# Kernel tuning notes

Measured on AMD Instinct MI355X. Metric: run time of the kernel, lower is better.

## Reference

```python
import jax, jax.numpy as jnp
import numpy as np

D_MODEL = 1024
N_HEADS = 16
HEAD_DIM = D_MODEL // N_HEADS


def setup_inputs() -> dict:
    key = jax.random.key(0)
    k1, k2, k3, k4, k5, k6 = jax.random.split(key, 6)
    B, T_q, T_kv = 4, 1024, 4096
    s = 1.0 / np.sqrt(D_MODEL)
    return {
        "query": jax.random.normal(k1, (B, T_q, D_MODEL), dtype=jnp.float32),
        "kv_source": jax.random.normal(k2, (B, T_kv, D_MODEL), dtype=jnp.float32),
        "w_q": jax.random.normal(k3, (D_MODEL, D_MODEL), dtype=jnp.float32) * s,
        "w_k": jax.random.normal(k4, (D_MODEL, D_MODEL), dtype=jnp.float32) * s,
        "w_v": jax.random.normal(k5, (D_MODEL, D_MODEL), dtype=jnp.float32) * s,
        "w_o": jax.random.normal(k6, (D_MODEL, D_MODEL), dtype=jnp.float32) * s,
    }


def reference(query, kv_source, w_q, w_k, w_v, w_o):
    B, T_q, _ = query.shape
    T_kv = kv_source.shape[1]
    # Linear(d,d,bias=False): y = x @ W^T
    q = (query @ w_q.T).reshape(B, T_q, N_HEADS, HEAD_DIM)
    k = (kv_source @ w_k.T).reshape(B, T_kv, N_HEADS, HEAD_DIM)
    v = (kv_source @ w_v.T).reshape(B, T_kv, N_HEADS, HEAD_DIM)
    scale = HEAD_DIM ** -0.5
    # scores: (B, H, T_q, T_kv)
    attn = jax.nn.softmax(jnp.einsum('bqhd,bkhd->bhqk', q, k) * scale, axis=-1)
    out = jnp.einsum('bhqk,bkhd->bqhd', attn, v).reshape(B, T_q, D_MODEL)
    return out @ w_o.T
```

## Files before the change

kernel.cpp:

```cpp
#include <hip/hip_runtime.h>
#include <hip/hip_bf16.h>


typedef __attribute__((ext_vector_type(4))) float f32x4;
typedef __attribute__((ext_vector_type(16))) float f32x16;
typedef __attribute__((ext_vector_type(8))) short bf16x8;

__device__ __forceinline__ unsigned short f2bf(float f) {
  unsigned u = __float_as_uint(f);
  u = (u + 0x7fffu + ((u >> 16) & 1u)) >> 16;
  return (unsigned short)u;
}

__device__ __forceinline__ void pl32swap(unsigned& x, unsigned& y) {
  asm volatile("v_permlane32_swap_b32 %0, %1" : "+v"(x), "+v"(y));
}

#define GLD_LDS16(g, l)                                                     \
  __builtin_amdgcn_global_load_lds(                                        \
      (const __attribute__((address_space(1))) unsigned int*)(const void*)(g), \
      (__attribute__((address_space(3))) unsigned int*)(void*)(l), 16, 0, 0)

__global__ void cvt_all(const float* __restrict__ q, const float* __restrict__ kv,
                        const float* __restrict__ wq, const float* __restrict__ wk,
                        const float* __restrict__ wv, const float* __restrict__ wo,
                        unsigned short* __restrict__ q_bf,
                        unsigned short* __restrict__ kv_bf,
                        unsigned short* __restrict__ wq_bf,
                        unsigned short* __restrict__ wk_bf,
                        unsigned short* __restrict__ wv_bf,
                        unsigned short* __restrict__ wo_bf) {
  const int QN = 4194304, KVN = 16777216, WN = 1048576;
  const float SC = 0.125f * 1.44269504088896f;
  int total_quads = (QN + KVN + 4 * WN) >> 2;
  int stride = gridDim.x * blockDim.x;
  for (int t = blockIdx.x * blockDim.x + threadIdx.x; t < total_quads; t += stride) {
    int i = t << 2;
    const float* src;
    unsigned short* dst;
    float sc = 1.0f;
    int off;
    if (i < QN) { src = q; dst = q_bf; off = i; }
    else if (i < QN + KVN) { src = kv; dst = kv_bf; off = i - QN; }
    else if (i < QN + KVN + WN) { src = wq; dst = wq_bf; off = i - QN - KVN; sc = SC; }
    else if (i < QN + KVN + 2 * WN) { src = wk; dst = wk_bf; off = i - QN - KVN - WN; }
    else if (i < QN + KVN + 3 * WN) { src = wv; dst = wv_bf; off = i - QN - KVN - 2 * WN; }
    else { src = wo; dst = wo_bf; off = i - QN - KVN - 3 * WN; }
    float4 v = *(const float4*)(src + off);
    ushort4 r;
    r.x = f2bf(v.x * sc); r.y = f2bf(v.y * sc);
    r.z = f2bf(v.z * sc); r.w = f2bf(v.w * sc);
    *(ushort4*)(dst + off) = r;
  }
}

template <int WRITE_BF16>
__global__ __launch_bounds__(256) void gemm_bt(
    const unsigned short* __restrict__ A, const unsigned short* __restrict__ Bt,
    void* __restrict__ Cp, int M, int N, int K, int ldc) {
  __shared__ __align__(16) unsigned short Ash[4096];
  __shared__ __align__(16) unsigned short Bsh[4096];

  int tiles_n = N >> 7;
  int nwg = gridDim.x;
  int wg = blockIdx.x;
  int cpx = nwg >> 3;
  wg = (wg & 7) * cpx + (wg >> 3);
  int tm = wg / tiles_n, tn = wg - tm * tiles_n;

  int tid = threadIdx.x;
  int lane = tid & 63, wave = tid >> 6;
  int wr = wave >> 1, wc = wave & 1;
  int brow = tm << 7, bcol = tn << 7;

  int fr = lane & 15, fg = lane >> 4;
  int swz = (fr >> 1) & 3;

  int srow = lane >> 2;
  int sg = (lane & 3) ^ ((srow >> 1) & 3);

  const unsigned short* aG0 = A + (size_t)(brow + wave * 32 + srow) * K + sg * 8;
  const unsigned short* aG1 = A + (size_t)(brow + wave * 32 + 16 + srow) * K + sg * 8;
  const unsigned short* bG0 = Bt + (size_t)(bcol + wave * 32 + srow) * K + sg * 8;
  const unsigned short* bG1 = Bt + (size_t)(bcol + wave * 32 + 16 + srow) * K + sg * 8;
  unsigned short* aL0 = Ash + wave * 1024;
  unsigned short* aL1 = Ash + wave * 1024 + 512;
  unsigned short* bL0 = Bsh + wave * 1024;
  unsigned short* bL1 = Bsh + wave * 1024 + 512;

  const f32x4 zero4 = {0.f, 0.f, 0.f, 0.f};
  f32x4 acc[4][4];
#pragma unroll
  for (int m = 0; m < 4; ++m)
#pragma unroll
    for (int n = 0; n < 4; ++n) acc[m][n] = zero4;

  for (int k0 = 0; k0 < K; k0 += 32) {
    GLD_LDS16(aG0 + k0, aL0);
    GLD_LDS16(aG1 + k0, aL1);
    GLD_LDS16(bG0 + k0, bL0);
    GLD_LDS16(bG1 + k0, bL1);
    __syncthreads();

    bf16x8 af[4], bfr[4];
#pragma unroll
    for (int m = 0; m < 4; ++m) {
      int r = wr * 64 + m * 16 + fr;
      af[m] = *(const bf16x8*)(Ash + r * 32 + ((fg ^ swz) * 8));
    }
#pragma unroll
    for (int n = 0; n < 4; ++n) {
      int r = wc * 64 + n * 16 + fr;
      bfr[n] = *(const bf16x8*)(Bsh + r * 32 + ((fg ^ swz) * 8));
    }
#pragma unroll
    for (int m = 0; m < 4; ++m)
#pragma unroll
      for (int n = 0; n < 4; ++n)
        acc[m][n] =
            __builtin_amdgcn_mfma_f32_16x16x32_bf16(af[m], bfr[n], acc[m][n], 0, 0, 0);
    __syncthreads();
  }

  int crow = brow + wr * 64 + fg * 4;
  int ccol = bcol + wc * 64 + fr;
#pragma unroll
  for (int m = 0; m < 4; ++m)
#pragma unroll
    for (int n = 0; n < 4; ++n)
#pragma unroll
      for (int j = 0; j < 4; ++j) {
        size_t off = (size_t)(crow + m * 16 + j) * ldc + (ccol + n * 16);
        if (WRITE_BF16)
          ((unsigned short*)Cp)[off] = f2bf(acc[m][n][j]);
        else
          ((float*)Cp)[off] = acc[m][n][j];
      }
}

__global__ __launch_bounds__(128) void attn_fwd(
    const unsigned short* __restrict__ qp,
    const unsigned short* __restrict__ kp,
    const unsigned short* __restrict__ vt,
    unsigned short* __restrict__ ao) {
  __shared__ __align__(16) unsigned short Ksh[128 * 64];
  __shared__ __align__(16) unsigned short Vsh[64 * 128];

  int idx = (blockIdx.x & 7) * 128 + (blockIdx.x >> 3);
  int qt = idx & 15;
  int h = (idx >> 4) & 15;
  int b = idx >> 8;
  int tid = threadIdx.x;
  int lane = tid & 63, w = tid >> 6;
  int q5 = lane & 31, hi = lane >> 5;

  const unsigned short* qptr =
      qp + (size_t)(b * 1024 + qt * 64 + w * 32 + q5) * 1024 + h * 64 + hi * 8;
  bf16x8 qf[4];
#pragma unroll
  for (int s = 0; s < 4; ++s) qf[s] = *(const bf16x8*)(qptr + s * 16);

  bf16x8 ones;
#pragma unroll
  for (int e = 0; e < 8; ++e) ones[e] = (short)0x3F80;

  f32x16 O[2], rsum;
#pragma unroll
  for (int r = 0; r < 16; ++r) { O[0][r] = 0.f; O[1][r] = 0.f; rsum[r] = 0.f; }
  float mrun = -1e30f;

  const unsigned short* kS[8];
#pragma unroll
  for (int i = 0; i < 8; ++i) {
    int row = w * 64 + i * 8 + (lane >> 3);
    int g = (lane & 7) ^ ((row ^ (2 * (row >> 3))) & 7);
    kS[i] = kp + (size_t)(b * 4096 + row) * 1024 + h * 64 + g * 8;
  }
  const unsigned short* vS[8];
#pragma unroll
  for (int i = 0; i < 8; ++i) {
    int row = w * 32 + i * 4 + (lane >> 4);
    int g = (lane & 15) ^ ((row >> 1) & 14);
    vS[i] = vt + (size_t)(h * 64 + row) * 16384 + b * 4096 + g * 8;
  }

  int xk = hi ^ ((q5 ^ (2 * (q5 >> 3))) & 7);
  int koff[4];
#pragma unroll
  for (int s = 0; s < 4; ++s) koff[s] = q5 * 64 + (((2 * s) ^ xk) * 8);
  int xv = hi ^ ((q5 >> 1) & 14);
  int voff[4][2];
#pragma unroll
  for (int kt = 0; kt < 4; ++kt)
#pragma unroll
    for (int p = 0; p < 2; ++p)
      voff[kt][p] = q5 * 128 + (((4 * kt + 2 * p) ^ xv) * 8);

  for (int it = 0; it < 32; ++it) {
#pragma unroll
    for (int i = 0; i < 8; ++i) GLD_LDS16(kS[i], Ksh + w * 4096 + i * 512);
#pragma unroll
    for (int i = 0; i < 8; ++i) GLD_LDS16(vS[i], Vsh + w * 4096 + i * 512);
#pragma unroll
    for (int i = 0; i < 8; ++i) { kS[i] += 131072; vS[i] += 128; }
    __syncthreads();

    f32x16 S[4];
#pragma unroll
    for (int kt = 0; kt < 4; ++kt)
#pragma unroll
      for (int r = 0; r < 16; ++r) S[kt][r] = 0.f;
    __builtin_amdgcn_s_setprio(1);
#pragma unroll
    for (int kt = 0; kt < 4; ++kt)
#pragma unroll
      for (int s = 0; s < 4; ++s) {
        bf16x8 kf = *(const bf16x8*)(Ksh + kt * 2048 + koff[s]);
        S[kt] = __builtin_amdgcn_mfma_f32_32x32x16_bf16(kf, qf[s], S[kt], 0, 0, 0);
      }
    __builtin_amdgcn_s_setprio(0);

    float t[16];
#pragma unroll
    for (int r = 0; r < 16; ++r)
      t[r] = fmaxf(fmaxf(S[0][r], S[1][r]), fmaxf(S[2][r], S[3][r]));
#pragma unroll
    for (int st = 8; st >= 1; st >>= 1)
#pragma unroll
      for (int r = 0; r < 8; ++r)
        if (r < st) t[r] = fmaxf(t[r], t[r + st]);
    float cmax = fmaxf(t[0], __shfl_xor(t[0], 32));

    if (__any(cmax > mrun)) {
      float mn = fmaxf(mrun, cmax);
      float fsc = exp2f(mrun - mn);
      mrun = mn;
#pragma unroll
      for (int r = 0; r < 16; ++r) {
        rsum[r] *= fsc; O[0][r] *= fsc; O[1][r] *= fsc;
      }
    }

#pragma unroll
    for (int kt = 0; kt < 4; ++kt) {
      float p[16];
#pragma unroll
      for (int r = 0; r < 16; ++r) p[r] = exp2f(S[kt][r] - mrun);
      unsigned u[8];
#pragma unroll
      for (int i = 0; i < 8; ++i) {
        __hip_bfloat162 pk = __float22bfloat162_rn(float2{p[2 * i], p[2 * i + 1]});
        u[i] = *reinterpret_cast<unsigned*>(&pk);
      }
      pl32swap(u[0], u[2]);
      pl32swap(u[1], u[3]);
      pl32swap(u[4], u[6]);
      pl32swap(u[5], u[7]);
      union PU { unsigned uu[4]; bf16x8 v; };
      PU a0; a0.uu[0] = u[0]; a0.uu[1] = u[1]; a0.uu[2] = u[2]; a0.uu[3] = u[3];
      PU a1; a1.uu[0] = u[4]; a1.uu[1] = u[5]; a1.uu[2] = u[6]; a1.uu[3] = u[7];
      bf16x8 pf0 = a0.v, pf1 = a1.v;

      __builtin_amdgcn_s_setprio(1);
      rsum = __builtin_amdgcn_mfma_f32_32x32x16_bf16(ones, pf0, rsum, 0, 0, 0);
      rsum = __builtin_amdgcn_mfma_f32_32x32x16_bf16(ones, pf1, rsum, 0, 0, 0);
#pragma unroll
      for (int dt = 0; dt < 2; ++dt) {
        bf16x8 vf0 = *(const bf16x8*)(Vsh + voff[kt][0] + dt * 4096);
        bf16x8 vf1 = *(const bf16x8*)(Vsh + voff[kt][1] + dt * 4096);
        O[dt] = __builtin_amdgcn_mfma_f32_32x32x16_bf16(vf0, pf0, O[dt], 0, 0, 0);
        O[dt] = __builtin_amdgcn_mfma_f32_32x32x16_bf16(vf1, pf1, O[dt], 0, 0, 0);
      }
      __builtin_amdgcn_s_setprio(0);
    }
    __syncthreads();
  }

  float inv = 1.0f / rsum[0];
  size_t obase = (size_t)(b * 1024 + qt * 64 + w * 32 + q5) * 1024 + h * 64;
#pragma unroll
  for (int dt = 0; dt < 2; ++dt)
#pragma unroll
    for (int j2 = 0; j2 < 4; ++j2) {
      ushort4 pk;
      pk.x = f2bf(O[dt][4 * j2 + 0] * inv);
      pk.y = f2bf(O[dt][4 * j2 + 1] * inv);
      pk.z = f2bf(O[dt][4 * j2 + 2] * inv);
      pk.w = f2bf(O[dt][4 * j2 + 3] * inv);
      *(ushort4*)(ao + obase + dt * 32 + j2 * 8 + hi * 4) = pk;
    }
}

extern "C" void kernel_launch(void* const* d_in, const int* in_sizes, int n_in,
                              void* d_out, int out_size, void* d_ws, size_t ws_size,
                              hipStream_t stream) {
  const float* query = (const float*)d_in[0];
  const float* kvs = (const float*)d_in[1];
  const float* wq = (const float*)d_in[2];
  const float* wk = (const float*)d_in[3];
  const float* wv = (const float*)d_in[4];
  const float* wo = (const float*)d_in[5];
  float* out = (float*)d_out;
  char* ws = (char*)d_ws;
  const size_t MB = 1ull << 20;

  unsigned short* q_bf = (unsigned short*)(ws + 0 * MB);
  unsigned short* kv_bf = (unsigned short*)(ws + 8 * MB);
  unsigned short* wq_bf = (unsigned short*)(ws + 40 * MB);
  unsigned short* wk_bf = (unsigned short*)(ws + 42 * MB);
  unsigned short* wv_bf = (unsigned short*)(ws + 44 * MB);
  unsigned short* wo_bf = (unsigned short*)(ws + 46 * MB);
  unsigned short* qp = (unsigned short*)(ws + 48 * MB);
  unsigned short* kp = (unsigned short*)(ws + 56 * MB);
  unsigned short* vt = (unsigned short*)(ws + 88 * MB);
  unsigned short* ao = (unsigned short*)(ws + 120 * MB);

  cvt_all<<<2048, 256, 0, stream>>>(query, kvs, wq, wk, wv, wo, q_bf, kv_bf,
                                    wq_bf, wk_bf, wv_bf, wo_bf);

  gemm_bt<1><<<256, 256, 0, stream>>>(q_bf, wq_bf, qp, 4096, 1024, 1024, 1024);
  gemm_bt<1><<<1024, 256, 0, stream>>>(kv_bf, wk_bf, kp, 16384, 1024, 1024, 1024);
  gemm_bt<1><<<1024, 256, 0, stream>>>(wv_bf, kv_bf, vt, 1024, 16384, 1024, 16384);

  attn_fwd<<<1024, 128, 0, stream>>>(qp, kp, vt, ao);

  gemm_bt<0><<<256, 256, 0, stream>>>(ao, wo_bf, out, 4096, 1024, 1024, 1024);
}
```

Measured before the change: 500.6 us.

## Split KV sequence across wave pairs in attention and merge partial softmax

The attention kernel now runs 4 waves per block instead of 2. Each pair of waves handles half of the KV sequence (split-K) for the same 64 queries, using 64-row KV tiles per iteration. The two partial softmax states are combined at the end through shared memory using the running max and sum. This raises occupancy and shortens the per-wave serial loop, at the cost of an extra LDS reduction and a barrier in the epilogue.

```diff
diff --git a/kernel.cpp b/kernel.cpp
--- a/kernel.cpp
+++ b/kernel.cpp
@@ -138,13 +138,14 @@
       }
 }
 
-__global__ __launch_bounds__(128) void attn_fwd(
+__global__ __launch_bounds__(256, 4) void attn_fwd(
     const unsigned short* __restrict__ qp,
     const unsigned short* __restrict__ kp,
     const unsigned short* __restrict__ vt,
     unsigned short* __restrict__ ao) {
-  __shared__ __align__(16) unsigned short Ksh[128 * 64];
-  __shared__ __align__(16) unsigned short Vsh[64 * 128];
+  __shared__ __align__(16) unsigned short SMEM[16384];
+  unsigned short* Ksh = SMEM;
+  unsigned short* Vsh = SMEM + 8192;
 
   int idx = (blockIdx.x & 7) * 128 + (blockIdx.x >> 3);
   int qt = idx & 15;
@@ -152,10 +153,11 @@
   int b = idx >> 8;
   int tid = threadIdx.x;
   int lane = tid & 63, w = tid >> 6;
+  int qsub = w & 1, kvh = w >> 1;
   int q5 = lane & 31, hi = lane >> 5;
 
   const unsigned short* qptr =
-      qp + (size_t)(b * 1024 + qt * 64 + w * 32 + q5) * 1024 + h * 64 + hi * 8;
+      qp + (size_t)(b * 1024 + qt * 64 + qsub * 32 + q5) * 1024 + h * 64 + hi * 8;
   bf16x8 qf[4];
 #pragma unroll
   for (int s = 0; s < 4; ++s) qf[s] = *(const bf16x8*)(qptr + s * 16);
@@ -164,131 +166,153 @@
 #pragma unroll
   for (int e = 0; e < 8; ++e) ones[e] = (short)0x3F80;
 
-  f32x16 O[2], rsum;
-#pragma unroll
-  for (int r = 0; r < 16; ++r) { O[0][r] = 0.f; O[1][r] = 0.f; rsum[r] = 0.f; }
+  f32x16 O0, O1, rsum;
+#pragma unroll
+  for (int r = 0; r < 16; ++r) { O0[r] = 0.f; O1[r] = 0.f; rsum[r] = 0.f; }
   float mrun = -1e30f;
 
-  const unsigned short* kS[8];
-#pragma unroll
-  for (int i = 0; i < 8; ++i) {
-    int row = w * 64 + i * 8 + (lane >> 3);
-    int g = (lane & 7) ^ ((row ^ (2 * (row >> 3))) & 7);
-    kS[i] = kp + (size_t)(b * 4096 + row) * 1024 + h * 64 + g * 8;
-  }
-  const unsigned short* vS[8];
-#pragma unroll
-  for (int i = 0; i < 8; ++i) {
-    int row = w * 32 + i * 4 + (lane >> 4);
-    int g = (lane & 15) ^ ((row >> 1) & 14);
-    vS[i] = vt + (size_t)(h * 64 + row) * 16384 + b * 4096 + g * 8;
-  }
-
-  int xk = hi ^ ((q5 ^ (2 * (q5 >> 3))) & 7);
-  int koff[4];
-#pragma unroll
-  for (int s = 0; s < 4; ++s) koff[s] = q5 * 64 + (((2 * s) ^ xk) * 8);
-  int xv = hi ^ ((q5 >> 1) & 14);
-  int voff[4][2];
-#pragma unroll
-  for (int kt = 0; kt < 4; ++kt)
-#pragma unroll
-    for (int p = 0; p < 2; ++p)
-      voff[kt][p] = q5 * 128 + (((4 * kt + 2 * p) ^ xv) * 8);
+  int lx = (lane & 7) ^ hi;
+  int srow = lane >> 3;
+  const unsigned short* kbase =
+      kp + (size_t)(b * 4096 + kvh * 2048 + qsub * 32 + srow) * 1024 + h * 64;
+  const unsigned short* vbase =
+      vt + (size_t)(h * 64 + qsub * 32 + srow) * 16384 + b * 4096 + kvh * 2048;
+  unsigned short* kdst = Ksh + kvh * 4096 + qsub * 2048;
+  unsigned short* vdst = Vsh + kvh * 4096 + qsub * 2048;
+
+  int hm = hi ^ ((q5 >> 2) & 7);
+  int soff[4];
+#pragma unroll
+  for (int c2 = 0; c2 < 4; ++c2) soff[c2] = ((2 * c2) ^ hm) * 8;
+  const unsigned short* kr = Ksh + kvh * 4096 + q5 * 64;
+  const unsigned short* vr = Vsh + kvh * 4096 + q5 * 64;
 
   for (int it = 0; it < 32; ++it) {
-#pragma unroll
-    for (int i = 0; i < 8; ++i) GLD_LDS16(kS[i], Ksh + w * 4096 + i * 512);
-#pragma unroll
-    for (int i = 0; i < 8; ++i) GLD_LDS16(vS[i], Vsh + w * 4096 + i * 512);
-#pragma unroll
-    for (int i = 0; i < 8; ++i) { kS[i] += 131072; vS[i] += 128; }
+    size_t kadv = (size_t)it * 65536;
+    int vadv = it * 64;
+#pragma unroll
+    for (int i = 0; i < 4; ++i) {
+      int gs = (lx ^ ((2 * i) & 7)) * 8;
+      GLD_LDS16(kbase + kadv + i * 8192 + gs, kdst + i * 512);
+      GLD_LDS16(vbase + vadv + (size_t)i * 131072 + gs, vdst + i * 512);
+    }
     __syncthreads();
 
-    f32x16 S[4];
-#pragma unroll
-    for (int kt = 0; kt < 4; ++kt)
-#pragma unroll
-      for (int r = 0; r < 16; ++r) S[kt][r] = 0.f;
+    f32x16 S0, S1;
+#pragma unroll
+    for (int r = 0; r < 16; ++r) { S0[r] = 0.f; S1[r] = 0.f; }
     __builtin_amdgcn_s_setprio(1);
 #pragma unroll
-    for (int kt = 0; kt < 4; ++kt)
-#pragma unroll
-      for (int s = 0; s < 4; ++s) {
-        bf16x8 kf = *(const bf16x8*)(Ksh + kt * 2048 + koff[s]);
-        S[kt] = __builtin_amdgcn_mfma_f32_32x32x16_bf16(kf, qf[s], S[kt], 0, 0, 0);
-      }
+    for (int s = 0; s < 4; ++s) {
+      bf16x8 kf0 = *(const bf16x8*)(kr + soff[s]);
+      bf16x8 kf1 = *(const bf16x8*)(kr + 2048 + soff[s]);
+      S0 = __builtin_amdgcn_mfma_f32_32x32x16_bf16(kf0, qf[s], S0, 0, 0, 0);
+      S1 = __builtin_amdgcn_mfma_f32_32x32x16_bf16(kf1, qf[s], S1, 0, 0, 0);
+    }
     __builtin_amdgcn_s_setprio(0);
 
-    float t[16];
-#pragma unroll
-    for (int r = 0; r < 16; ++r)
-      t[r] = fmaxf(fmaxf(S[0][r], S[1][r]), fmaxf(S[2][r], S[3][r]));
-#pragma unroll
-    for (int st = 8; st >= 1; st >>= 1)
-#pragma unroll
-      for (int r = 0; r < 8; ++r)
-        if (r < st) t[r] = fmaxf(t[r], t[r + st]);
-    float cmax = fmaxf(t[0], __shfl_xor(t[0], 32));
+    float ta[8];
+#pragma unroll
+    for (int j = 0; j < 8; ++j)
+      ta[j] = fmaxf(fmaxf(S0[j], S0[j + 8]), fmaxf(S1[j], S1[j + 8]));
+    float c0 = fmaxf(fmaxf(ta[0], ta[4]), fmaxf(ta[1], ta[5]));
+    float c1 = fmaxf(fmaxf(ta[2], ta[6]), fmaxf(ta[3], ta[7]));
+    float cmax = fmaxf(c0, c1);
+    cmax = fmaxf(cmax, __shfl_xor(cmax, 32));
 
     if (__any(cmax > mrun)) {
       float mn = fmaxf(mrun, cmax);
       float fsc = exp2f(mrun - mn);
       mrun = mn;
-#pragma unroll
-      for (int r = 0; r < 16; ++r) {
-        rsum[r] *= fsc; O[0][r] *= fsc; O[1][r] *= fsc;
-      }
-    }
-
-#pragma unroll
-    for (int kt = 0; kt < 4; ++kt) {
-      float p[16];
-#pragma unroll
-      for (int r = 0; r < 16; ++r) p[r] = exp2f(S[kt][r] - mrun);
-      unsigned u[8];
-#pragma unroll
-      for (int i = 0; i < 8; ++i) {
-        __hip_bfloat162 pk = __float22bfloat162_rn(float2{p[2 * i], p[2 * i + 1]});
-        u[i] = *reinterpret_cast<unsigned*>(&pk);
-      }
-      pl32swap(u[0], u[2]);
-      pl32swap(u[1], u[3]);
-      pl32swap(u[4], u[6]);
-      pl32swap(u[5], u[7]);
-      union PU { unsigned uu[4]; bf16x8 v; };
-      PU a0; a0.uu[0] = u[0]; a0.uu[1] = u[1]; a0.uu[2] = u[2]; a0.uu[3] = u[3];
-      PU a1; a1.uu[0] = u[4]; a1.uu[1] = u[5]; a1.uu[2] = u[6]; a1.uu[3] = u[7];
-      bf16x8 pf0 = a0.v, pf1 = a1.v;
-
-      __builtin_amdgcn_s_setprio(1);
-      rsum = __builtin_amdgcn_mfma_f32_32x32x16_bf16(ones, pf0, rsum, 0, 0, 0);
-      rsum = __builtin_amdgcn_mfma_f32_32x32x16_bf16(ones, pf1, rsum, 0, 0, 0);
-#pragma unroll
-      for (int dt = 0; dt < 2; ++dt) {
-        bf16x8 vf0 = *(const bf16x8*)(Vsh + voff[kt][0] + dt * 4096);
-        bf16x8 vf1 = *(const bf16x8*)(Vsh + voff[kt][1] + dt * 4096);
-        O[dt] = __builtin_amdgcn_mfma_f32_32x32x16_bf16(vf0, pf0, O[dt], 0, 0, 0);
-        O[dt] = __builtin_amdgcn_mfma_f32_32x32x16_bf16(vf1, pf1, O[dt], 0, 0, 0);
-      }
-      __builtin_amdgcn_s_setprio(0);
-    }
+      rsum[0] *= fsc;
+#pragma unroll
+      for (int r = 0; r < 16; ++r) { O0[r] *= fsc; O1[r] *= fsc; }
+    }
+
+#define PACK_PV(SK, KT)                                                       \
+    {                                                                         \
+      _Pragma("unroll")                                                       \
+      for (int r = 0; r < 16; ++r) SK[r] = exp2f(SK[r] - mrun);               \
+      unsigned u[8];                                                          \
+      _Pragma("unroll")                                                       \
+      for (int i2 = 0; i2 < 8; ++i2) {                                        \
+        __hip_bfloat162 pk =                                                  \
+            __float22bfloat162_rn(float2{SK[2 * i2], SK[2 * i2 + 1]});        \
+        u[i2] = *reinterpret_cast<unsigned*>(&pk);                            \
+      }                                                                       \
+      pl32swap(u[0], u[2]); pl32swap(u[1], u[3]);                             \
+      pl32swap(u[4], u[6]); pl32swap(u[5], u[7]);                             \
+      union PU { unsigned uu[4]; bf16x8 v; };                                 \
+      PU a0; a0.uu[0] = u[0]; a0.uu[1] = u[1]; a0.uu[2] = u[2]; a0.uu[3] = u[3]; \
+      PU a1; a1.uu[0] = u[4]; a1.uu[1] = u[5]; a1.uu[2] = u[6]; a1.uu[3] = u[7]; \
+      bf16x8 pf0 = a0.v, pf1 = a1.v;                                          \
+      __builtin_amdgcn_s_setprio(1);                                          \
+      rsum = __builtin_amdgcn_mfma_f32_32x32x16_bf16(ones, pf0, rsum, 0, 0, 0); \
+      rsum = __builtin_amdgcn_mfma_f32_32x32x16_bf16(ones, pf1, rsum, 0, 0, 0); \
+      bf16x8 vf;                                                              \
+      vf = *(const bf16x8*)(vr + soff[2 * KT + 0]);                           \
+      O0 = __builtin_amdgcn_mfma_f32_32x32x16_bf16(vf, pf0, O0, 0, 0, 0);     \
+      vf = *(const bf16x8*)(vr + soff[2 * KT + 1]);                           \
+      O0 = __builtin_amdgcn_mfma_f32_32x32x16_bf16(vf, pf1, O0, 0, 0, 0);     \
+      vf = *(const bf16x8*)(vr + 2048 + soff[2 * KT + 0]);                    \
+      O1 = __builtin_amdgcn_mfma_f32_32x32x16_bf16(vf, pf0, O1, 0, 0, 0);     \
+      vf = *(const bf16x8*)(vr + 2048 + soff[2 * KT + 1]);                    \
+      O1 = __builtin_amdgcn_mfma_f32_32x32x16_bf16(vf, pf1, O1, 0, 0, 0);     \
+      __builtin_amdgcn_s_setprio(0);                                          \
+    }
+
+    PACK_PV(S0, 0)
+    PACK_PV(S1, 1)
+#undef PACK_PV
+
     __syncthreads();
   }
 
-  float inv = 1.0f / rsum[0];
-  size_t obase = (size_t)(b * 1024 + qt * 64 + w * 32 + q5) * 1024 + h * 64;
-#pragma unroll
-  for (int dt = 0; dt < 2; ++dt)
-#pragma unroll
-    for (int j2 = 0; j2 < 4; ++j2) {
+  float* fb = (float*)SMEM;
+  float* bm = fb + 4352;
+  float* bs = fb + 4416;
+  int qrow_l = qsub * 32 + q5;
+  if (kvh == 1) {
+    float* rowp = fb + qrow_l * 68;
+#pragma unroll
+    for (int r = 0; r < 16; ++r) {
+      int d = (r & 3) + 8 * (r >> 2) + 4 * hi;
+      rowp[d] = O0[r];
+      rowp[32 + d] = O1[r];
+    }
+    bm[qrow_l] = mrun;
+    bs[qrow_l] = rsum[0];
+  }
+  __syncthreads();
+  if (kvh == 0) {
+    float m2 = bm[qrow_l], s2 = bs[qrow_l];
+    float ms = fmaxf(mrun, m2);
+    float f1 = exp2f(mrun - ms), f2 = exp2f(m2 - ms);
+    float inv = 1.0f / (rsum[0] * f1 + s2 * f2);
+    f1 *= inv; f2 *= inv;
+    float* rowp = fb + qrow_l * 68;
+    size_t obase = (size_t)(b * 1024 + qt * 64 + qrow_l) * 1024 + h * 64;
+#pragma unroll
+    for (int c = 0; c < 4; ++c) {
+      f32x4 o2 = *(const f32x4*)(rowp + 8 * c + 4 * hi);
       ushort4 pk;
-      pk.x = f2bf(O[dt][4 * j2 + 0] * inv);
-      pk.y = f2bf(O[dt][4 * j2 + 1] * inv);
-      pk.z = f2bf(O[dt][4 * j2 + 2] * inv);
-      pk.w = f2bf(O[dt][4 * j2 + 3] * inv);
-      *(ushort4*)(ao + obase + dt * 32 + j2 * 8 + hi * 4) = pk;
-    }
+      pk.x = f2bf(O0[4 * c + 0] * f1 + o2[0] * f2);
+      pk.y = f2bf(O0[4 * c + 1] * f1 + o2[1] * f2);
+      pk.z = f2bf(O0[4 * c + 2] * f1 + o2[2] * f2);
+      pk.w = f2bf(O0[4 * c + 3] * f1 + o2[3] * f2);
+      *(ushort4*)(ao + obase + c * 8 + hi * 4) = pk;
+    }
+#pragma unroll
+    for (int c = 0; c < 4; ++c) {
+      f32x4 o2 = *(const f32x4*)(rowp + 32 + 8 * c + 4 * hi);
+      ushort4 pk;
+      pk.x = f2bf(O1[4 * c + 0] * f1 + o2[0] * f2);
+      pk.y = f2bf(O1[4 * c + 1] * f1 + o2[1] * f2);
+      pk.z = f2bf(O1[4 * c + 2] * f1 + o2[2] * f2);
+      pk.w = f2bf(O1[4 * c + 3] * f1 + o2[3] * f2);
+      *(ushort4*)(ao + obase + 32 + c * 8 + hi * 4) = pk;
+    }
+  }
 }
 
 extern "C" void kernel_launch(void* const* d_in, const int* in_sizes, int n_in,
@@ -322,7 +346,7 @@
   gemm_bt<1><<<1024, 256, 0, stream>>>(kv_bf, wk_bf, kp, 16384, 1024, 1024, 1024);
   gemm_bt<1><<<1024, 256, 0, stream>>>(wv_bf, kv_bf, vt, 1024, 16384, 1024, 16384);
 
-  attn_fwd<<<1024, 128, 0, stream>>>(qp, kp, vt, ao);
+  attn_fwd<<<1024, 256, 0, stream>>>(qp, kp, vt, ao);
 
   gemm_bt<0><<<256, 256, 0, stream>>>(ao, wo_bf, out, 4096, 1024, 1024, 1024);
 }
```

New measurement: 445.8 us. -10.9%, faster.

## Double-buffer K/V tiles in attention and double queries per block

Applied to the files above, without the earlier changes.

The attention kernel now uses 256-thread blocks covering 128 queries, so each K/V tile loaded into LDS is shared by four waves instead of two. The single-buffered K/V staging with a sync before compute becomes a double-buffered pipeline that prefetches the next tile while the current one is processed, and the LDS swizzle patterns are simplified. The aim is to hide global-to-LDS latency and halve K/V load traffic per query. The cost is double the LDS (64KB per block), which may lower occupancy, and only 512 blocks on the grid.

```diff
diff --git a/kernel.cpp b/kernel.cpp
--- a/kernel.cpp
+++ b/kernel.cpp
@@ -138,24 +138,23 @@
       }
 }
 
-__global__ __launch_bounds__(128) void attn_fwd(
+__global__ __launch_bounds__(256) void attn_fwd(
     const unsigned short* __restrict__ qp,
     const unsigned short* __restrict__ kp,
     const unsigned short* __restrict__ vt,
     unsigned short* __restrict__ ao) {
-  __shared__ __align__(16) unsigned short Ksh[128 * 64];
-  __shared__ __align__(16) unsigned short Vsh[64 * 128];
-
-  int idx = (blockIdx.x & 7) * 128 + (blockIdx.x >> 3);
-  int qt = idx & 15;
-  int h = (idx >> 4) & 15;
-  int b = idx >> 8;
+  __shared__ __align__(16) unsigned short SMEM[32768];
+
+  int idx = (blockIdx.x & 7) * 64 + (blockIdx.x >> 3);
+  int qt = idx & 7;
+  int h = (idx >> 3) & 15;
+  int b = idx >> 7;
   int tid = threadIdx.x;
   int lane = tid & 63, w = tid >> 6;
   int q5 = lane & 31, hi = lane >> 5;
 
   const unsigned short* qptr =
-      qp + (size_t)(b * 1024 + qt * 64 + w * 32 + q5) * 1024 + h * 64 + hi * 8;
+      qp + (size_t)(b * 1024 + qt * 128 + w * 32 + q5) * 1024 + h * 64 + hi * 8;
   bf16x8 qf[4];
 #pragma unroll
   for (int s = 0; s < 4; ++s) qf[s] = *(const bf16x8*)(qptr + s * 16);
@@ -164,46 +163,47 @@
 #pragma unroll
   for (int e = 0; e < 8; ++e) ones[e] = (short)0x3F80;
 
-  f32x16 O[2], rsum;
-#pragma unroll
-  for (int r = 0; r < 16; ++r) { O[0][r] = 0.f; O[1][r] = 0.f; rsum[r] = 0.f; }
+  f32x16 O0, O1, rsum;
+#pragma unroll
+  for (int r = 0; r < 16; ++r) { O0[r] = 0.f; O1[r] = 0.f; rsum[r] = 0.f; }
   float mrun = -1e30f;
 
-  const unsigned short* kS[8];
-#pragma unroll
-  for (int i = 0; i < 8; ++i) {
-    int row = w * 64 + i * 8 + (lane >> 3);
-    int g = (lane & 7) ^ ((row ^ (2 * (row >> 3))) & 7);
-    kS[i] = kp + (size_t)(b * 4096 + row) * 1024 + h * 64 + g * 8;
-  }
-  const unsigned short* vS[8];
-#pragma unroll
-  for (int i = 0; i < 8; ++i) {
-    int row = w * 32 + i * 4 + (lane >> 4);
-    int g = (lane & 15) ^ ((row >> 1) & 14);
-    vS[i] = vt + (size_t)(h * 64 + row) * 16384 + b * 4096 + g * 8;
-  }
-
-  int xk = hi ^ ((q5 ^ (2 * (q5 >> 3))) & 7);
+  int gk = (tid & 7) ^ ((tid >> 3) & 7);
+  const unsigned short* kS =
+      kp + (size_t)(b * 4096 + (tid >> 3)) * 1024 + h * 64 + gk * 8;
+  int gv = (tid & 15) ^ ((tid >> 4) & 7);
+  const unsigned short* vS =
+      vt + (size_t)(h * 64 + (tid >> 4)) * 16384 + b * 4096 + gv * 8;
+
+  int hx = hi ^ (q5 & 7);
   int koff[4];
 #pragma unroll
-  for (int s = 0; s < 4; ++s) koff[s] = q5 * 64 + (((2 * s) ^ xk) * 8);
-  int xv = hi ^ ((q5 >> 1) & 14);
-  int voff[4][2];
-#pragma unroll
-  for (int kt = 0; kt < 4; ++kt)
-#pragma unroll
-    for (int p = 0; p < 2; ++p)
-      voff[kt][p] = q5 * 128 + (((4 * kt + 2 * p) ^ xv) * 8);
+  for (int s = 0; s < 4; ++s) koff[s] = q5 * 64 + (((2 * s) ^ hx) * 8);
+  int voff[8];
+#pragma unroll
+  for (int s = 0; s < 8; ++s) voff[s] = (((2 * s) ^ hx) * 8);
+
+#define STAGE(buf, kadv, vadv)                                                \
+  {                                                                           \
+    _Pragma("unroll")                                                         \
+    for (int i = 0; i < 4; ++i) {                                             \
+      GLD_LDS16(kS + (kadv) + i * 32768, (buf) + i * 2048 + w * 512);         \
+      GLD_LDS16(vS + (vadv) + i * 262144, (buf) + 8192 + i * 2048 + w * 512); \
+    }                                                                         \
+  }
+
+  STAGE(SMEM, 0, 0);
+  __syncthreads();
 
   for (int it = 0; it < 32; ++it) {
-#pragma unroll
-    for (int i = 0; i < 8; ++i) GLD_LDS16(kS[i], Ksh + w * 4096 + i * 512);
-#pragma unroll
-    for (int i = 0; i < 8; ++i) GLD_LDS16(vS[i], Vsh + w * 4096 + i * 512);
-#pragma unroll
-    for (int i = 0; i < 8; ++i) { kS[i] += 131072; vS[i] += 128; }
-    __syncthreads();
+    const unsigned short* cur = SMEM + (it & 1) * 16384;
+    if (it < 31) {
+      unsigned short* nxt = SMEM + ((it + 1) & 1) * 16384;
+      STAGE(nxt, (size_t)(it + 1) * 131072, (it + 1) * 128);
+    }
+
+    const unsigned short* Kb = cur;
+    const unsigned short* Vb = cur + 8192;
 
     f32x16 S[4];
 #pragma unroll
@@ -215,30 +215,28 @@
     for (int kt = 0; kt < 4; ++kt)
 #pragma unroll
       for (int s = 0; s < 4; ++s) {
-        bf16x8 kf = *(const bf16x8*)(Ksh + kt * 2048 + koff[s]);
+        bf16x8 kf = *(const bf16x8*)(Kb + kt * 2048 + koff[s]);
         S[kt] = __builtin_amdgcn_mfma_f32_32x32x16_bf16(kf, qf[s], S[kt], 0, 0, 0);
       }
     __builtin_amdgcn_s_setprio(0);
 
-    float t[16];
+    float tm[16];
 #pragma unroll
     for (int r = 0; r < 16; ++r)
-      t[r] = fmaxf(fmaxf(S[0][r], S[1][r]), fmaxf(S[2][r], S[3][r]));
+      tm[r] = fmaxf(fmaxf(S[0][r], S[1][r]), fmaxf(S[2][r], S[3][r]));
 #pragma unroll
     for (int st = 8; st >= 1; st >>= 1)
 #pragma unroll
-      for (int r = 0; r < 8; ++r)
-        if (r < st) t[r] = fmaxf(t[r], t[r + st]);
-    float cmax = fmaxf(t[0], __shfl_xor(t[0], 32));
+      for (int r = 0; r < st; ++r) tm[r] = fmaxf(tm[r], tm[r + st]);
+    float cmax = fmaxf(tm[0], __shfl_xor(tm[0], 32));
 
     if (__any(cmax > mrun)) {
       float mn = fmaxf(mrun, cmax);
       float fsc = exp2f(mrun - mn);
       mrun = mn;
-#pragma unroll
-      for (int r = 0; r < 16; ++r) {
-        rsum[r] *= fsc; O[0][r] *= fsc; O[1][r] *= fsc;
-      }
+      rsum[0] *= fsc;
+#pragma unroll
+      for (int r = 0; r < 16; ++r) { O0[r] *= fsc; O1[r] *= fsc; }
     }
 
 #pragma unroll
@@ -248,14 +246,13 @@
       for (int r = 0; r < 16; ++r) p[r] = exp2f(S[kt][r] - mrun);
       unsigned u[8];
 #pragma unroll
-      for (int i = 0; i < 8; ++i) {
-        __hip_bfloat162 pk = __float22bfloat162_rn(float2{p[2 * i], p[2 * i + 1]});
-        u[i] = *reinterpret_cast<unsigned*>(&pk);
+      for (int i2 = 0; i2 < 8; ++i2) {
+        __hip_bfloat162 pk =
+            __float22bfloat162_rn(float2{p[2 * i2], p[2 * i2 + 1]});
+        u[i2] = *reinterpret_cast<unsigned*>(&pk);
       }
-      pl32swap(u[0], u[2]);
-      pl32swap(u[1], u[3]);
-      pl32swap(u[4], u[6]);
-      pl32swap(u[5], u[7]);
+      pl32swap(u[0], u[2]); pl32swap(u[1], u[3]);
+      pl32swap(u[4], u[6]); pl32swap(u[5], u[7]);
       union PU { unsigned uu[4]; bf16x8 v; };
       PU a0; a0.uu[0] = u[0]; a0.uu[1] = u[1]; a0.uu[2] = u[2]; a0.uu[3] = u[3];
       PU a1; a1.uu[0] = u[4]; a1.uu[1] = u[5]; a1.uu[2] = u[6]; a1.uu[3] = u[7];
@@ -264,31 +261,42 @@
       __builtin_amdgcn_s_setprio(1);
       rsum = __builtin_amdgcn_mfma_f32_32x32x16_bf16(ones, pf0, rsum, 0, 0, 0);
       rsum = __builtin_amdgcn_mfma_f32_32x32x16_bf16(ones, pf1, rsum, 0, 0, 0);
-#pragma unroll
-      for (int dt = 0; dt < 2; ++dt) {
-        bf16x8 vf0 = *(const bf16x8*)(Vsh + voff[kt][0] + dt * 4096);
-        bf16x8 vf1 = *(const bf16x8*)(Vsh + voff[kt][1] + dt * 4096);
-        O[dt] = __builtin_amdgcn_mfma_f32_32x32x16_bf16(vf0, pf0, O[dt], 0, 0, 0);
-        O[dt] = __builtin_amdgcn_mfma_f32_32x32x16_bf16(vf1, pf1, O[dt], 0, 0, 0);
-      }
+      bf16x8 vf;
+      vf = *(const bf16x8*)(Vb + q5 * 128 + voff[2 * kt + 0]);
+      O0 = __builtin_amdgcn_mfma_f32_32x32x16_bf16(vf, pf0, O0, 0, 0, 0);
+      vf = *(const bf16x8*)(Vb + q5 * 128 + voff[2 * kt + 1]);
+      O0 = __builtin_amdgcn_mfma_f32_32x32x16_bf16(vf, pf1, O0, 0, 0, 0);
+      vf = *(const bf16x8*)(Vb + 4096 + q5 * 128 + voff[2 * kt + 0]);
+      O1 = __builtin_amdgcn_mfma_f32_32x32x16_bf16(vf, pf0, O1, 0, 0, 0);
+      vf = *(const bf16x8*)(Vb + 4096 + q5 * 128 + voff[2 * kt + 1]);
+      O1 = __builtin_amdgcn_mfma_f32_32x32x16_bf16(vf, pf1, O1, 0, 0, 0);
       __builtin_amdgcn_s_setprio(0);
     }
+
     __syncthreads();
   }
+#undef STAGE
 
   float inv = 1.0f / rsum[0];
-  size_t obase = (size_t)(b * 1024 + qt * 64 + w * 32 + q5) * 1024 + h * 64;
-#pragma unroll
-  for (int dt = 0; dt < 2; ++dt)
-#pragma unroll
-    for (int j2 = 0; j2 < 4; ++j2) {
-      ushort4 pk;
-      pk.x = f2bf(O[dt][4 * j2 + 0] * inv);
-      pk.y = f2bf(O[dt][4 * j2 + 1] * inv);
-      pk.z = f2bf(O[dt][4 * j2 + 2] * inv);
-      pk.w = f2bf(O[dt][4 * j2 + 3] * inv);
-      *(ushort4*)(ao + obase + dt * 32 + j2 * 8 + hi * 4) = pk;
-    }
+  size_t obase = (size_t)(b * 1024 + qt * 128 + w * 32 + q5) * 1024 + h * 64;
+#pragma unroll
+  for (int j2 = 0; j2 < 4; ++j2) {
+    ushort4 pk;
+    pk.x = f2bf(O0[4 * j2 + 0] * inv);
+    pk.y = f2bf(O0[4 * j2 + 1] * inv);
+    pk.z = f2bf(O0[4 * j2 + 2] * inv);
+    pk.w = f2bf(O0[4 * j2 + 3] * inv);
+    *(ushort4*)(ao + obase + j2 * 8 + hi * 4) = pk;
+  }
+#pragma unroll
+  for (int j2 = 0; j2 < 4; ++j2) {
+    ushort4 pk;
+    pk.x = f2bf(O1[4 * j2 + 0] * inv);
+    pk.y = f2bf(O1[4 * j2 + 1] * inv);
+    pk.z = f2bf(O1[4 * j2 + 2] * inv);
+    pk.w = f2bf(O1[4 * j2 + 3] * inv);
+    *(ushort4*)(ao + obase + 32 + j2 * 8 + hi * 4) = pk;
+  }
 }
 
 extern "C" void kernel_launch(void* const* d_in, const int* in_sizes, int n_in,
@@ -322,7 +330,7 @@
   gemm_bt<1><<<1024, 256, 0, stream>>>(kv_bf, wk_bf, kp, 16384, 1024, 1024, 1024);
   gemm_bt<1><<<1024, 256, 0, stream>>>(wv_bf, kv_bf, vt, 1024, 16384, 1024, 16384);
 
-  attn_fwd<<<1024, 128, 0, stream>>>(qp, kp, vt, ao);
+  attn_fwd<<<512, 256, 0, stream>>>(qp, kp, vt, ao);
 
   gemm_bt<0><<<256, 256, 0, stream>>>(ao, wo_bf, out, 4096, 1024, 1024, 1024);
 }
```

After: 479.7 us. -4.2%, faster.
